# Kernel optimization log

Measured on AMD Instinct MI355X. Metric: run time of the kernel, lower is better.

## Reference

```python
import jax, jax.numpy as jnp
import numpy as np

Q_DIM = 4096
K_DIM = 4096  # used only for the 1/sqrt(k_dim) scale


def setup_inputs() -> dict:
    key = jax.random.key(0)
    k1, k2, k3 = jax.random.split(key, 3)
    queries = jax.random.normal(k1, (4096, Q_DIM), dtype=jnp.float32)  # (N, q_dim)
    keys = jax.random.normal(k2, (4096, 8192), dtype=jnp.float32)      # (N, M)
    values = jax.random.normal(k3, (4096, 8192), dtype=jnp.float32)    # (v_dim, M)
    return {"queries": queries, "keys": keys, "values": values}


def reference(queries, keys, values):
    # queries.view(-1, q_dim).T -> (q_dim, N)
    q = queries.reshape(-1, Q_DIM).T
    # scores: (q_dim, M), scaled then softmax over M
    scores = (q @ keys) * (1.0 / np.sqrt(K_DIM).astype(np.float32))
    attn = jax.nn.softmax(scores, axis=-1)
    # values.T -> (M, v_dim); output: (q_dim, v_dim)
    return attn @ values.T
```

## Files before the change

kernel.cpp:

```cpp
#include <hip/hip_runtime.h>
#include <hip/hip_bf16.h>
#include <stdint.h>

using bf16 = __hip_bfloat16;
typedef __attribute__((ext_vector_type(8))) short  frag_ab;
typedef __attribute__((ext_vector_type(4))) float  frag_cd;

#define AS3(p)  ((__attribute__((address_space(3))) void*)(p))
#define AS1C(p) ((const __attribute__((address_space(1))) void*)(p))

static __device__ __forceinline__ float bf_to_f(unsigned short h) {
  union { unsigned u; float f; } c; c.u = ((unsigned)h) << 16; return c.f;
}
static __device__ __forceinline__ unsigned short f_to_bf(float f) {
  union { float fv; unsigned u; } c; c.fv = f;
  unsigned u = c.u + (0x7FFFu + ((c.u >> 16) & 1u));
  return (unsigned short)(u >> 16);
}

__global__ __launch_bounds__(256)
void transpose_cast_kernel(const float* __restrict__ in,
                           unsigned short* __restrict__ out,
                           int R, int C) {
  __shared__ float tile[64][65];
  const int t = threadIdx.x;
  const size_t c0 = (size_t)blockIdx.x * 64;
  const size_t r0 = (size_t)blockIdx.y * 64;
  const int lr = t >> 4;
  const int lc = (t & 15) * 4;
  #pragma unroll
  for (int i = 0; i < 64; i += 16) {
    const float4 v = *(const float4*)(in + (r0 + lr + i) * C + (c0 + lc));
    tile[lr + i][lc]     = v.x;
    tile[lr + i][lc + 1] = v.y;
    tile[lr + i][lc + 2] = v.z;
    tile[lr + i][lc + 3] = v.w;
  }
  __syncthreads();
  const int oc = t >> 3;
  const int orr = (t & 7) * 8;
  #pragma unroll
  for (int p = 0; p < 2; ++p) {
    const int c = oc + p * 32;
    frag_ab o;
    #pragma unroll
    for (int j = 0; j < 8; ++j) o[j] = (short)f_to_bf(tile[orr + j][c]);
    *(frag_ab*)(out + (c0 + c) * R + (r0 + orr)) = o;
  }
}

__global__ void cast_kernel(const float* __restrict__ in, unsigned short* __restrict__ out) {
  const size_t i = ((size_t)blockIdx.x * 256 + threadIdx.x) * 8;
  const float4 a = *(const float4*)(in + i);
  const float4 b = *(const float4*)(in + i + 4);
  frag_ab o;
  o[0] = (short)f_to_bf(a.x); o[1] = (short)f_to_bf(a.y);
  o[2] = (short)f_to_bf(a.z); o[3] = (short)f_to_bf(a.w);
  o[4] = (short)f_to_bf(b.x); o[5] = (short)f_to_bf(b.y);
  o[6] = (short)f_to_bf(b.z); o[7] = (short)f_to_bf(b.w);
  *(frag_ab*)(out + i) = o;
}

template <bool OUT_BF16>
__global__ __launch_bounds__(512)
void gemm256_kernel(const bf16* __restrict__ A, const bf16* __restrict__ B,
                    void* __restrict__ Cv, int N, int K, float scale,
                    int nbx, int nby) {
  __shared__ __align__(16) bf16 sA[2][2][128 * 64];
  __shared__ __align__(16) bf16 sB[2][2][128 * 64];

  const int t    = threadIdx.x;
  const int lane = t & 63;
  const int wv   = t >> 6;
  const int wm   = wv >> 2;
  const int wn   = wv & 3;

  const int nb  = nbx * nby;
  const int bid = blockIdx.x;
  const int u   = (bid & 7) * (nb >> 3) + (bid >> 3);
  const int GM = 4;
  const int width = GM * nbx;
  const int gid = u / width;
  const int pm  = gid * GM + (u % GM);
  const int pn  = (u % width) / GM;
  const size_t bm = (size_t)pm * 256;
  const size_t bn = (size_t)pn * 256;

  const int r0 = t >> 3;
  const int cg = (t & 7) ^ (r0 & 7);
  const bf16* gA = A + (bm + (size_t)r0) * K + cg * 8;
  const bf16* gB = B + (bn + (size_t)r0) * K + cg * 8;
  const size_t hstep = (size_t)128 * K;
  const size_t lstep = (size_t)64  * K;

  const int mf   = lane & 15;
  const int quad = lane >> 4;
  const int swz  = mf & 7;
  const int ck0  = ((0 * 4 + quad) ^ swz) * 8;
  const int ck1  = ((1 * 4 + quad) ^ swz) * 8;
  const int aoff = (wm * 64 + mf) * 64;
  const int boff = (wn * 32 + mf) * 64;

  frag_cd acc[8][4];
  #pragma unroll
  for (int i = 0; i < 8; ++i)
    #pragma unroll
    for (int j = 0; j < 4; ++j)
      acc[i][j] = (frag_cd){0.f, 0.f, 0.f, 0.f};

  frag_ab ar[8];
  frag_ab b0[4];
  frag_ab b1[4];

#define STG(arr, g, bufi, half, kt) do {                                          \
    __builtin_amdgcn_global_load_lds(AS1C((g) + (half) * hstep + (kt)),           \
                                     AS3(&arr[bufi][half][t * 8]), 16, 0, 0);     \
    __builtin_amdgcn_global_load_lds(AS1C((g) + (half) * hstep + lstep + (kt)),   \
                                     AS3(&arr[bufi][half][(512 + t) * 8]), 16, 0, 0); \
  } while (0)

#define LDA(bufi, mh) do {                                                        \
    _Pragma("unroll") for (int mi = 0; mi < 4; ++mi) {                            \
      ar[mi * 2 + 0] = *(const frag_ab*)(&sA[bufi][mh][0] + aoff + mi * 1024 + ck0); \
      ar[mi * 2 + 1] = *(const frag_ab*)(&sA[bufi][mh][0] + aoff + mi * 1024 + ck1); \
    } } while (0)

#define LDB(dst, bufi, nh) do {                                                   \
    _Pragma("unroll") for (int ni = 0; ni < 2; ++ni) {                            \
      dst[ni * 2 + 0] = *(const frag_ab*)(&sB[bufi][nh][0] + boff + ni * 1024 + ck0); \
      dst[ni * 2 + 1] = *(const frag_ab*)(&sB[bufi][nh][0] + boff + ni * 1024 + ck1); \
    } } while (0)

#define MM(mh, nh, bb) do {                                                       \
    __builtin_amdgcn_s_setprio(1);                                                \
    _Pragma("unroll") for (int mi = 0; mi < 4; ++mi)                              \
      _Pragma("unroll") for (int ni = 0; ni < 2; ++ni)                            \
        _Pragma("unroll") for (int kk = 0; kk < 2; ++kk)                          \
          acc[(mh) * 4 + mi][(nh) * 2 + ni] = __builtin_amdgcn_mfma_f32_16x16x32_bf16( \
              ar[mi * 2 + kk], bb[ni * 2 + kk], acc[(mh) * 4 + mi][(nh) * 2 + ni], 0, 0, 0); \
    __builtin_amdgcn_s_setprio(0);                                                \
  } while (0)

#define BAR() do { asm volatile("" ::: "memory");                                 \
                   __builtin_amdgcn_s_barrier();                                  \
                   asm volatile("" ::: "memory"); } while (0)
#define WAIT4() asm volatile("s_waitcnt vmcnt(4)" ::: "memory")

  STG(sA, gA, 0, 0, 0);
  STG(sB, gB, 0, 0, 0);
  STG(sA, gA, 0, 1, 0);
  STG(sB, gB, 0, 1, 0);
  STG(sA, gA, 1, 0, 64);
  STG(sB, gB, 1, 1, 64);
  WAIT4();
  BAR();

  const int NIT = K >> 7;
  for (int i = 0; i < NIT; ++i) {
    const int k1 = i * 128 + 64;
    const int last = (i == NIT - 1);
    const int k2 = last ? 0 : i * 128 + 128;
    const int k3 = last ? 0 : i * 128 + 192;

    LDA(0, 0); LDB(b0, 0, 0);
    STG(sA, gA, 1, 1, k1);
    BAR(); MM(0, 0, b0); BAR();
    LDB(b1, 0, 1);
    STG(sB, gB, 1, 0, k1);
    BAR(); MM(0, 1, b1); BAR();
    LDA(0, 1);
    STG(sA, gA, 0, 0, k2);
    BAR(); MM(1, 1, b1); BAR();
    STG(sB, gB, 0, 1, k2);
    BAR(); MM(1, 0, b0);
    WAIT4(); BAR();
    LDA(1, 0); LDB(b0, 1, 0);
    STG(sA, gA, 0, 1, k2);
    BAR(); MM(0, 0, b0); BAR();
    LDB(b1, 1, 1);
    STG(sB, gB, 0, 0, k2);
    BAR(); MM(0, 1, b1); BAR();
    LDA(1, 1);
    STG(sA, gA, 1, 0, k3);
    BAR(); MM(1, 1, b1); BAR();
    STG(sB, gB, 1, 1, k3);
    BAR(); MM(1, 0, b0);
    WAIT4(); BAR();
  }

#undef STG
#undef LDA
#undef LDB
#undef MM
#undef BAR
#undef WAIT4

  #pragma unroll
  for (int m8 = 0; m8 < 8; ++m8) {
    const int mh = m8 >> 2, mi = m8 & 3;
    const size_t mbase = bm + mh * 128 + wm * 64 + mi * 16 + quad * 4;
    #pragma unroll
    for (int n4 = 0; n4 < 4; ++n4) {
      const int nh = n4 >> 1, ni = n4 & 1;
      const size_t n = bn + nh * 128 + wn * 32 + ni * 16 + mf;
      #pragma unroll
      for (int r = 0; r < 4; ++r) {
        const float v = acc[m8][n4][r] * scale;
        const size_t idx = (mbase + r) * (size_t)N + n;
        if (OUT_BF16) ((unsigned short*)Cv)[idx] = f_to_bf(v);
        else          ((float*)Cv)[idx] = v;
      }
    }
  }
}

__global__ __launch_bounds__(256)
void softmax_kernel(unsigned short* __restrict__ S) {
  unsigned short* row = S + (size_t)blockIdx.x * 8192;
  const int tid = threadIdx.x;
  const int wv = tid >> 6, ln = tid & 63;
  __shared__ float red[8];

  float x[32];
  #pragma unroll
  for (int c = 0; c < 4; ++c) {
    frag_ab v = *(const frag_ab*)(row + c * 2048 + tid * 8);
    #pragma unroll
    for (int j = 0; j < 8; ++j) x[c * 8 + j] = bf_to_f((unsigned short)v[j]);
  }
  float mx = x[0];
  #pragma unroll
  for (int i = 1; i < 32; ++i) mx = fmaxf(mx, x[i]);
  #pragma unroll
  for (int off = 32; off >= 1; off >>= 1) mx = fmaxf(mx, __shfl_xor(mx, off, 64));
  if (ln == 0) red[wv] = mx;
  __syncthreads();
  mx = fmaxf(fmaxf(red[0], red[1]), fmaxf(red[2], red[3]));

  float s = 0.f;
  #pragma unroll
  for (int i = 0; i < 32; ++i) { x[i] = __expf(x[i] - mx); s += x[i]; }
  #pragma unroll
  for (int off = 32; off >= 1; off >>= 1) s += __shfl_xor(s, off, 64);
  if (ln == 0) red[4 + wv] = s;
  __syncthreads();
  const float inv = 1.f / ((red[4] + red[5]) + (red[6] + red[7]));

  #pragma unroll
  for (int c = 0; c < 4; ++c) {
    frag_ab o;
    #pragma unroll
    for (int j = 0; j < 8; ++j) o[j] = (short)f_to_bf(x[c * 8 + j] * inv);
    *(frag_ab*)(row + c * 2048 + tid * 8) = o;
  }
}

extern "C" void kernel_launch(void* const* d_in, const int* in_sizes, int n_in,
                              void* d_out, int out_size, void* d_ws, size_t ws_size,
                              hipStream_t stream) {
  const float* Q  = (const float*)d_in[0];
  const float* Km = (const float*)d_in[1];
  const float* V  = (const float*)d_in[2];
  float* O = (float*)d_out;

  const int Nc = 4096;
  const int QD = 4096;
  const int M  = 8192;
  const int VD = 4096;

  bf16* Qt = (bf16*)d_ws;
  bf16* Kt = Qt + (size_t)QD * Nc;
  bf16* Vb = Kt + (size_t)M * Nc;
  bf16* Sb = Vb + (size_t)VD * M;

  transpose_cast_kernel<<<dim3(QD / 64, Nc / 64), 256, 0, stream>>>(
      Q, (unsigned short*)Qt, Nc, QD);
  transpose_cast_kernel<<<dim3(M / 64, Nc / 64), 256, 0, stream>>>(
      Km, (unsigned short*)Kt, Nc, M);
  cast_kernel<<<(int)(((size_t)VD * M) / (256 * 8)), 256, 0, stream>>>(
      V, (unsigned short*)Vb);

  gemm256_kernel<true><<<(M / 256) * (QD / 256), 512, 0, stream>>>(
      Qt, Kt, (void*)Sb, M, Nc, 0.015625f, M / 256, QD / 256);
  softmax_kernel<<<QD, 256, 0, stream>>>((unsigned short*)Sb);
  gemm256_kernel<false><<<(VD / 256) * (QD / 256), 512, 0, stream>>>(
      Sb, Vb, (void*)O, VD, M, 1.0f, VD / 256, QD / 256);
}
```

Baseline: 791.5 us.

## Reschedule GEMM main loop to halve barriers and prefetch fragments across phases

```diff
diff --git a/kernel.cpp b/kernel.cpp
--- a/kernel.cpp
+++ b/kernel.cpp
@@ -144,7 +144,7 @@
 #define BAR() do { asm volatile("" ::: "memory");                                 \
                    __builtin_amdgcn_s_barrier();                                  \
                    asm volatile("" ::: "memory"); } while (0)
-#define WAIT4() asm volatile("s_waitcnt vmcnt(4)" ::: "memory")
+#define WAITN(n) asm volatile("s_waitcnt vmcnt(" #n ")" ::: "memory")
 
   STG(sA, gA, 0, 0, 0);
   STG(sB, gB, 0, 0, 0);
@@ -152,8 +152,9 @@
   STG(sB, gB, 0, 1, 0);
   STG(sA, gA, 1, 0, 64);
   STG(sB, gB, 1, 1, 64);
-  WAIT4();
+  WAITN(4);
   BAR();
+  LDA(0, 0); LDB(b0, 0, 0);
 
   const int NIT = K >> 7;
   for (int i = 0; i < NIT; ++i) {
@@ -162,30 +163,40 @@
     const int k2 = last ? 0 : i * 128 + 128;
     const int k3 = last ? 0 : i * 128 + 192;
 
+    STG(sB, gB, 1, 0, k1);
+    MM(0, 0, b0);
+    LDB(b1, 0, 1);
+    WAITN(6);
+    BAR();
+    STG(sA, gA, 1, 1, k1);
+    MM(0, 1, b1);
+    LDA(0, 1);
+    BAR();
+    STG(sA, gA, 0, 0, k2);
+    MM(1, 1, b1);
+    WAITN(4);
+    BAR();
+    STG(sB, gB, 0, 1, k2);
+    MM(1, 0, b0);
+    LDA(1, 0); LDB(b0, 1, 0);
+    BAR();
+    STG(sB, gB, 0, 0, k2);
+    MM(0, 0, b0);
+    LDB(b1, 1, 1);
+    WAITN(6);
+    BAR();
+    STG(sA, gA, 0, 1, k2);
+    MM(0, 1, b1);
+    LDA(1, 1);
+    BAR();
+    STG(sA, gA, 1, 0, k3);
+    MM(1, 1, b1);
+    WAITN(4);
+    BAR();
+    STG(sB, gB, 1, 1, k3);
+    MM(1, 0, b0);
     LDA(0, 0); LDB(b0, 0, 0);
-    STG(sA, gA, 1, 1, k1);
-    BAR(); MM(0, 0, b0); BAR();
-    LDB(b1, 0, 1);
-    STG(sB, gB, 1, 0, k1);
-    BAR(); MM(0, 1, b1); BAR();
-    LDA(0, 1);
-    STG(sA, gA, 0, 0, k2);
-    BAR(); MM(1, 1, b1); BAR();
-    STG(sB, gB, 0, 1, k2);
-    BAR(); MM(1, 0, b0);
-    WAIT4(); BAR();
-    LDA(1, 0); LDB(b0, 1, 0);
-    STG(sA, gA, 0, 1, k2);
-    BAR(); MM(0, 0, b0); BAR();
-    LDB(b1, 1, 1);
-    STG(sB, gB, 0, 0, k2);
-    BAR(); MM(0, 1, b1); BAR();
-    LDA(1, 1);
-    STG(sA, gA, 1, 0, k3);
-    BAR(); MM(1, 1, b1); BAR();
-    STG(sB, gB, 1, 1, k3);
-    BAR(); MM(1, 0, b0);
-    WAIT4(); BAR();
+    BAR();
   }
 
 #undef STG
@@ -193,7 +204,7 @@
 #undef LDB
 #undef MM
 #undef BAR
-#undef WAIT4
+#undef WAITN
 
   #pragma unroll
   for (int m8 = 0; m8 < 8; ++m8) {
```

Result: no change. 802.9 us (+1.5%).
